# Kernel tuning notes

Measured on AMD Instinct MI355X. Metric: run time of the kernel, lower is better.

Reference implementation:

```python
import jax, jax.numpy as jnp
import numpy as np

N_NODES = 10000
N_EDGES = 640000
N_GRAPHS = 64
IN_FEAT = 128
HID = (128, 128)
NUM_CLASS = 10


def setup_inputs() -> dict:
    key = jax.random.key(0)
    ks = jax.random.split(key, 10)
    x = jax.random.normal(ks[0], (N_NODES, IN_FEAT), dtype=jnp.float32)
    edge_index = jax.random.randint(ks[1], (2, N_EDGES), 0, N_NODES, dtype=jnp.int64)
    batch = jnp.sort(jax.random.randint(ks[2], (N_NODES,), 0, N_GRAPHS, dtype=jnp.int64))
    # GCNConv weights (PyG applies x @ W then propagates, bias added after aggregation)
    s1 = 1.0 / np.sqrt(IN_FEAT)
    s2 = 1.0 / np.sqrt(HID[0])
    s3 = 1.0 / np.sqrt(HID[1])
    W1 = jax.random.uniform(ks[3], (IN_FEAT, HID[0]), jnp.float32, -s1, s1)
    b1 = jnp.zeros((HID[0],), jnp.float32)
    W2 = jax.random.uniform(ks[4], (HID[0], HID[1]), jnp.float32, -s2, s2)
    b2 = jnp.zeros((HID[1],), jnp.float32)
    Wlin = jax.random.uniform(ks[5], (HID[1], NUM_CLASS), jnp.float32, -s3, s3)
    blin = jax.random.uniform(ks[6], (NUM_CLASS,), jnp.float32, -s3, s3)
    return {"x": x, "edge_index": edge_index, "batch": batch,
            "W1": W1, "b1": b1, "W2": W2, "b2": b2, "Wlin": Wlin, "blin": blin}


def _gcn_conv(x, src, dst, W, b):
    # GCNConv with self-loops and symmetric normalization:
    # out[i] = sum_{(j->i) in E} d[j]^{-1/2} d[i]^{-1/2} (x_j W) + d[i]^{-1} (x_i W) + b
    # where d = in-degree (on dst) + 1 for the self-loop.
    h = x @ W                                                      # [N, F]
    ones = jnp.ones(src.shape[0], dtype=h.dtype)
    deg = jax.ops.segment_sum(ones, dst, num_segments=x.shape[0]) + 1.0
    dinv = jax.lax.rsqrt(deg)                                      # [N]
    norm = dinv[src] * dinv[dst]                                   # [E]
    agg = jax.ops.segment_sum(h[src] * norm[:, None], dst, num_segments=x.shape[0])
    agg = agg + h * (dinv * dinv)[:, None]                         # self-loop term
    return agg + b


def _global_mean_pool(x, batch, num_graphs):
    sums = jax.ops.segment_sum(x, batch, num_segments=num_graphs)          # [G, F]
    cnt = jax.ops.segment_sum(jnp.ones(x.shape[0], x.dtype), batch, num_segments=num_graphs)
    return sums / jnp.maximum(cnt, 1.0)[:, None]


def reference(x, edge_index, batch, W1, b1, W2, b2, Wlin, blin):
    src, dst = edge_index[0], edge_index[1]
    h = jax.nn.relu(_gcn_conv(x, src, dst, W1, b1))
    h = jax.nn.relu(_gcn_conv(h, src, dst, W2, b2))
    g = _global_mean_pool(h, batch, N_GRAPHS)      # [G, hid1]
    return g @ Wlin + blin                          # [G, num_class]
```

## Files before the change

kernel.cpp:

```cpp
#include <hip/hip_runtime.h>

#define NN 10000
#define NE 640000
#define NG 64
#define NF 128
#define NC 10
#define TMR 16
#define TKC 32
#define NB 250
#define BSZ 40
#define G1 512
#define GEMMB ((NN + TMR - 1) / TMR)
#define ECHUNK 1250
#define CAP 32
#define CCAP 3072
#define NSL 64
#define MAXD 192


__device__ __forceinline__ unsigned short f2bf(float f) {
    unsigned int u = __float_as_uint(f);
    return (unsigned short)((u + 0x7FFF + ((u >> 16) & 1)) >> 16);
}
__device__ __forceinline__ float bf_lo(unsigned int p) {
    return __uint_as_float(p << 16);
}
__device__ __forceinline__ float bf_hi(unsigned int p) {
    return __uint_as_float(p & 0xFFFF0000u);
}

__device__ __forceinline__ int detect64(const int* w, long span) {
    int lane = threadIdx.x & 63;
    long e = (long)lane * (span - 1) / 63;
    return (__ballot(w[2 * e + 1] != 0) == 0ULL) ? 1 : 0;
}

__device__ __forceinline__ int ld_idx(const void* p, long i, int is64) {
    return is64 ? (int)((const long long*)p)[i] : ((const int*)p)[i];
}

__global__ __launch_bounds__(256) void k_prepgemm(const void* __restrict__ ei,
                                                  const void* __restrict__ batch,
                                                  int* __restrict__ bh,
                                                  int* __restrict__ ebuf,
                                                  float* __restrict__ outacc,
                                                  float* __restrict__ cntinv,
                                                  const float* __restrict__ X,
                                                  const float* __restrict__ W,
                                                  unsigned short* __restrict__ Y) {
    __shared__ int hist[256];
    __shared__ int cur[256];
    __shared__ float sX[TKC * 20];
    __shared__ float sW[32 * 132];
    int tid = threadIdx.x;

    if (blockIdx.x >= G1) {
        int m0 = (int)(blockIdx.x - G1) * TMR;
        int rg = tid & 7;
        int cg = tid >> 3;
        float acc[2][4] = {{0.f}};
        for (int kc = 0; kc < NF / TKC; ++kc) {
            int k0 = kc * TKC;
            if (tid < 128) {
                int row = tid >> 3, kq = tid & 7;
                int mm = m0 + row; if (mm > NN - 1) mm = NN - 1;
                float4 v = *(const float4*)(X + (size_t)mm * NF + k0 + kq * 4);
                sX[(kq * 4 + 0) * 20 + row] = v.x;
                sX[(kq * 4 + 1) * 20 + row] = v.y;
                sX[(kq * 4 + 2) * 20 + row] = v.z;
                sX[(kq * 4 + 3) * 20 + row] = v.w;
            }
#pragma unroll
            for (int j = 0; j < 4; ++j) {
                int idx = tid + 256 * j;
                int k = idx >> 5, cq = idx & 31;
                float4 v = *(const float4*)(W + (size_t)(k0 + k) * NF + cq * 4);
                *(float4*)(sW + cq * 132 + k * 4) = v;
            }
            __syncthreads();
#pragma unroll 8
            for (int k = 0; k < TKC; ++k) {
                float2 xf = *(const float2*)(sX + k * 20 + rg * 2);
                float4 wf = *(const float4*)(sW + cg * 132 + k * 4);
                acc[0][0] = fmaf(xf.x, wf.x, acc[0][0]);
                acc[0][1] = fmaf(xf.x, wf.y, acc[0][1]);
                acc[0][2] = fmaf(xf.x, wf.z, acc[0][2]);
                acc[0][3] = fmaf(xf.x, wf.w, acc[0][3]);
                acc[1][0] = fmaf(xf.y, wf.x, acc[1][0]);
                acc[1][1] = fmaf(xf.y, wf.y, acc[1][1]);
                acc[1][2] = fmaf(xf.y, wf.z, acc[1][2]);
                acc[1][3] = fmaf(xf.y, wf.w, acc[1][3]);
            }
            __syncthreads();
        }
#pragma unroll
        for (int r = 0; r < 2; ++r) {
            int m = m0 + rg * 2 + r;
            if (m < NN) {
                ushort4 h;
                h.x = f2bf(acc[r][0]);
                h.y = f2bf(acc[r][1]);
                h.z = f2bf(acc[r][2]);
                h.w = f2bf(acc[r][3]);
                *(ushort4*)(Y + (size_t)m * NF + cg * 4) = h;
            }
        }
        return;
    }

    int is64 = detect64((const int*)ei, NE);
    hist[tid] = 0;
    __syncthreads();
    if (blockIdx.x == 0) {
        for (int i = tid; i < NSL * NG * NC; i += 256) outacc[i] = 0.f;
    }
    if (blockIdx.x == 8 && tid < NG) {
        int isb = detect64((const int*)batch, NN / 2);
        int lo0 = 0, hi0 = NN;
        while (lo0 < hi0) {
            int m = (lo0 + hi0) >> 1;
            if (ld_idx(batch, m, isb) < tid) lo0 = m + 1; else hi0 = m;
        }
        int lo1 = lo0, hi1 = NN;
        while (lo1 < hi1) {
            int m = (lo1 + hi1) >> 1;
            if (ld_idx(batch, m, isb) < tid + 1) lo1 = m + 1; else hi1 = m;
        }
        cntinv[tid] = 1.0f / fmaxf((float)(lo1 - lo0), 1.0f);
    }
    int e0 = blockIdx.x * ECHUNK;
    int dstv[5], srcv[5];
#pragma unroll
    for (int i = 0; i < 5; ++i) {
        int r = tid + i * 256;
        if (r < ECHUNK) {
            long e = (long)e0 + r;
            dstv[i] = ld_idx(ei, (long)NE + e, is64);
            srcv[i] = ld_idx(ei, e, is64);
            atomicAdd(&hist[dstv[i] / BSZ], 1);
        } else {
            dstv[i] = -1; srcv[i] = 0;
        }
    }
    __syncthreads();
    if (tid < NB) {
        bh[tid * G1 + blockIdx.x] = min(hist[tid], CAP);
        cur[tid] = (tid * G1 + blockIdx.x) * CAP;
    }
    __syncthreads();
#pragma unroll
    for (int i = 0; i < 5; ++i) {
        if (tid + i * 256 < ECHUNK) {
            int dst = dstv[i], src = srcv[i];
            int b = dst / BSZ;
            int p = atomicAdd(&cur[b], 1);
            int lim = (b * G1 + blockIdx.x) * CAP + CAP;
            if (p < lim) ebuf[p] = ((dst - b * BSZ) << 14) | src;
        }
    }
}

__global__ __launch_bounds__(256) void k_csr(const int* __restrict__ ebuf,
                                             const int* __restrict__ bh,
                                             int* __restrict__ coff,
                                             int* __restrict__ deg,
                                             float* __restrict__ dinv,
                                             unsigned short* __restrict__ csrc) {
    __shared__ int scnt[G1];
    __shared__ int cbase[G1];
    __shared__ int wsum[4];
    __shared__ int eb[CCAP];
    __shared__ int dcount[BSZ];
    __shared__ int cur[BSZ];
    int b = blockIdx.x, tid = threadIdx.x;
    int lane = tid & 63, wv = tid >> 6;
    for (int i = tid; i < G1; i += 256) scnt[i] = bh[b * G1 + i];
    if (tid < BSZ) dcount[tid] = 0;
    __syncthreads();
    int v0 = scnt[2 * tid], v1 = scnt[2 * tid + 1];
    int lsum = v0 + v1;
    int pref = lsum;
    for (int o = 1; o < 64; o <<= 1) {
        int t = __shfl_up(pref, o, 64);
        if (lane >= o) pref += t;
    }
    if (lane == 63) wsum[wv] = pref;
    __syncthreads();
    int off = 0;
#pragma unroll
    for (int j = 0; j < 4; ++j) if (j < wv) off += wsum[j];
    int ex = pref - lsum + off;
    cbase[2 * tid] = ex;
    cbase[2 * tid + 1] = ex + v0;
    int tot = wsum[0] + wsum[1] + wsum[2] + wsum[3];
    if (tot > CCAP) tot = CCAP;
    __syncthreads();
#pragma unroll
    for (int cp = 0; cp < 2; ++cp) {
        int cell = 2 * tid + cp;
        int c = scnt[cell], lb = cbase[cell];
        int gb = (b * G1 + cell) * CAP;
        if (lb + c > CCAP) c = max(0, CCAP - lb);
        for (int i = 0; i < c; ++i) eb[lb + i] = ebuf[gb + i];
    }
    __syncthreads();
    for (int i = tid; i < tot; i += 256)
        atomicAdd(&dcount[eb[i] >> 14], 1);
    __syncthreads();
    if (tid < 64) {
        int d = (tid < BSZ) ? dcount[tid] : 0;
        int pr = d;
        for (int o = 1; o < 64; o <<= 1) {
            int t = __shfl_up(pr, o, 64);
            if (tid >= o) pr += t;
        }
        if (tid < BSZ) {
            int st = pr - d;
            cur[tid] = b * CCAP + st;
            coff[b * BSZ + tid] = b * CCAP + st;
            deg[b * BSZ + tid] = d;
            dinv[b * BSZ + tid] = rsqrtf((float)d + 1.0f);
        }
    }
    __syncthreads();
    for (int i = tid; i < tot; i += 256) {
        int pk = eb[i];
        int p = atomicAdd(&cur[pk >> 14], 1);
        csrc[p] = (unsigned short)(pk & 16383);
    }
}

__global__ __launch_bounds__(256) void k_gemm(const float* __restrict__ X,
                                              const float* __restrict__ W,
                                              const float* __restrict__ dinv,
                                              unsigned short* __restrict__ Y,
                                              int nrows) {
    __shared__ float sX[TKC * 20];
    __shared__ float sW[32 * 132];
    int tid = threadIdx.x;
    int rg = tid & 7;
    int cg = tid >> 3;
    int m0 = blockIdx.x * TMR;
    float acc[2][4] = {{0.f}};
    for (int kc = 0; kc < NF / TKC; ++kc) {
        int k0 = kc * TKC;
        if (tid < 128) {
            int row = tid >> 3, kq = tid & 7;
            int mm = m0 + row; if (mm > nrows - 1) mm = nrows - 1;
            float4 v = *(const float4*)(X + (size_t)mm * NF + k0 + kq * 4);
            sX[(kq * 4 + 0) * 20 + row] = v.x;
            sX[(kq * 4 + 1) * 20 + row] = v.y;
            sX[(kq * 4 + 2) * 20 + row] = v.z;
            sX[(kq * 4 + 3) * 20 + row] = v.w;
        }
#pragma unroll
        for (int j = 0; j < 4; ++j) {
            int idx = tid + 256 * j;
            int k = idx >> 5, cq = idx & 31;
            float4 v = *(const float4*)(W + (size_t)(k0 + k) * NF + cq * 4);
            *(float4*)(sW + cq * 132 + k * 4) = v;
        }
        __syncthreads();
#pragma unroll 8
        for (int k = 0; k < TKC; ++k) {
            float2 xf = *(const float2*)(sX + k * 20 + rg * 2);
            float4 wf = *(const float4*)(sW + cg * 132 + k * 4);
            acc[0][0] = fmaf(xf.x, wf.x, acc[0][0]);
            acc[0][1] = fmaf(xf.x, wf.y, acc[0][1]);
            acc[0][2] = fmaf(xf.x, wf.z, acc[0][2]);
            acc[0][3] = fmaf(xf.x, wf.w, acc[0][3]);
            acc[1][0] = fmaf(xf.y, wf.x, acc[1][0]);
            acc[1][1] = fmaf(xf.y, wf.y, acc[1][1]);
            acc[1][2] = fmaf(xf.y, wf.z, acc[1][2]);
            acc[1][3] = fmaf(xf.y, wf.w, acc[1][3]);
        }
        __syncthreads();
    }
#pragma unroll
    for (int r = 0; r < 2; ++r) {
        int m = m0 + rg * 2 + r;
        if (m < nrows) {
            float ds = dinv[m];
            ushort4 h;
            h.x = f2bf(acc[r][0] * ds);
            h.y = f2bf(acc[r][1] * ds);
            h.z = f2bf(acc[r][2] * ds);
            h.w = f2bf(acc[r][3] * ds);
            *(ushort4*)(Y + (size_t)m * NF + cg * 4) = h;
        }
    }
}

template <int EDGE_SCALE>
__device__ __forceinline__ void gacc_node(const unsigned short* __restrict__ G,
                                          const unsigned short* __restrict__ csrc,
                                          const float* __restrict__ dv,
                                          unsigned short* ls, float* lsd,
                                          int beg, int end, int q, int f, int lane,
                                          float a[8]) {
    int dg = end - beg;
    int nst = min(dg, MAXD);
    for (int i = lane; i < nst; i += 64) {
        unsigned short s = csrc[beg + i];
        ls[i] = s;
        if (EDGE_SCALE) lsd[i] = dv[s];
    }
    int vi = q;
    int nfull = nst & ~31;
    for (; vi < nfull; vi += 32) {
        int s[8]; float d[8];
#pragma unroll
        for (int j = 0; j < 8; ++j) {
            s[j] = ls[vi + 4 * j];
            d[j] = EDGE_SCALE ? lsd[vi + 4 * j] : 1.f;
        }
        uint4 p[8];
#pragma unroll
        for (int j = 0; j < 8; ++j)
            p[j] = ((const uint4*)(G + (size_t)s[j] * NF))[f];
#pragma unroll
        for (int j = 0; j < 8; ++j) {
            if (EDGE_SCALE) {
                a[0] = fmaf(d[j], bf_lo(p[j].x), a[0]); a[1] = fmaf(d[j], bf_hi(p[j].x), a[1]);
                a[2] = fmaf(d[j], bf_lo(p[j].y), a[2]); a[3] = fmaf(d[j], bf_hi(p[j].y), a[3]);
                a[4] = fmaf(d[j], bf_lo(p[j].z), a[4]); a[5] = fmaf(d[j], bf_hi(p[j].z), a[5]);
                a[6] = fmaf(d[j], bf_lo(p[j].w), a[6]); a[7] = fmaf(d[j], bf_hi(p[j].w), a[7]);
            } else {
                a[0] += bf_lo(p[j].x); a[1] += bf_hi(p[j].x);
                a[2] += bf_lo(p[j].y); a[3] += bf_hi(p[j].y);
                a[4] += bf_lo(p[j].z); a[5] += bf_hi(p[j].z);
                a[6] += bf_lo(p[j].w); a[7] += bf_hi(p[j].w);
            }
        }
    }
    int nfull16 = nst & ~15;
    for (; vi < nfull16; vi += 16) {
        int s[4]; float d[4];
#pragma unroll
        for (int j = 0; j < 4; ++j) {
            s[j] = ls[vi + 4 * j];
            d[j] = EDGE_SCALE ? lsd[vi + 4 * j] : 1.f;
        }
        uint4 p[4];
#pragma unroll
        for (int j = 0; j < 4; ++j)
            p[j] = ((const uint4*)(G + (size_t)s[j] * NF))[f];
#pragma unroll
        for (int j = 0; j < 4; ++j) {
            if (EDGE_SCALE) {
                a[0] = fmaf(d[j], bf_lo(p[j].x), a[0]); a[1] = fmaf(d[j], bf_hi(p[j].x), a[1]);
                a[2] = fmaf(d[j], bf_lo(p[j].y), a[2]); a[3] = fmaf(d[j], bf_hi(p[j].y), a[3]);
                a[4] = fmaf(d[j], bf_lo(p[j].z), a[4]); a[5] = fmaf(d[j], bf_hi(p[j].z), a[5]);
                a[6] = fmaf(d[j], bf_lo(p[j].w), a[6]); a[7] = fmaf(d[j], bf_hi(p[j].w), a[7]);
            } else {
                a[0] += bf_lo(p[j].x); a[1] += bf_hi(p[j].x);
                a[2] += bf_lo(p[j].y); a[3] += bf_hi(p[j].y);
                a[4] += bf_lo(p[j].z); a[5] += bf_hi(p[j].z);
                a[6] += bf_lo(p[j].w); a[7] += bf_hi(p[j].w);
            }
        }
    }
    int npad = (nst + 3) & ~3;
    for (; vi < npad; vi += 4) {
        int ii = min(vi, nst - 1);
        int s = ls[ii];
        float d = EDGE_SCALE ? lsd[ii] : 1.f;
        uint4 p = ((const uint4*)(G + (size_t)s * NF))[f];
        if (vi < nst) {
            if (EDGE_SCALE) {
                a[0] = fmaf(d, bf_lo(p.x), a[0]); a[1] = fmaf(d, bf_hi(p.x), a[1]);
                a[2] = fmaf(d, bf_lo(p.y), a[2]); a[3] = fmaf(d, bf_hi(p.y), a[3]);
                a[4] = fmaf(d, bf_lo(p.z), a[4]); a[5] = fmaf(d, bf_hi(p.z), a[5]);
                a[6] = fmaf(d, bf_lo(p.w), a[6]); a[7] = fmaf(d, bf_hi(p.w), a[7]);
            } else {
                a[0] += bf_lo(p.x); a[1] += bf_hi(p.x);
                a[2] += bf_lo(p.y); a[3] += bf_hi(p.y);
                a[4] += bf_lo(p.z); a[5] += bf_hi(p.z);
                a[6] += bf_lo(p.w); a[7] += bf_hi(p.w);
            }
        }
    }
    for (int e2 = beg + MAXD + q; e2 < end; e2 += 4) {
        int s = csrc[e2];
        float d = EDGE_SCALE ? dv[s] : 1.f;
        uint4 p = ((const uint4*)(G + (size_t)s * NF))[f];
        if (EDGE_SCALE) {
            a[0] = fmaf(d, bf_lo(p.x), a[0]); a[1] = fmaf(d, bf_hi(p.x), a[1]);
            a[2] = fmaf(d, bf_lo(p.y), a[2]); a[3] = fmaf(d, bf_hi(p.y), a[3]);
            a[4] = fmaf(d, bf_lo(p.z), a[4]); a[5] = fmaf(d, bf_hi(p.z), a[5]);
            a[6] = fmaf(d, bf_lo(p.w), a[6]); a[7] = fmaf(d, bf_hi(p.w), a[7]);
        } else {
            a[0] += bf_lo(p.x); a[1] += bf_hi(p.x);
            a[2] += bf_lo(p.y); a[3] += bf_hi(p.y);
            a[4] += bf_lo(p.z); a[5] += bf_hi(p.z);
            a[6] += bf_lo(p.w); a[7] += bf_hi(p.w);
        }
    }
#pragma unroll
    for (int j = 0; j < 8; ++j) a[j] += __shfl_xor(a[j], 16);
#pragma unroll
    for (int j = 0; j < 8; ++j) a[j] += __shfl_xor(a[j], 32);
}

__global__ __launch_bounds__(256, 4) void k_gather(const unsigned short* __restrict__ G,
                                                   const int* __restrict__ off,
                                                   const int* __restrict__ dg,
                                                   const unsigned short* __restrict__ csrc,
                                                   const float* __restrict__ dinv,
                                                   const float* __restrict__ bias,
                                                   float* __restrict__ OUT) {
    __shared__ unsigned short lsbuf[4][MAXD];
    __shared__ float lsdbuf[4][MAXD];
    int wid = threadIdx.x >> 6, lane = threadIdx.x & 63;
    int q = lane >> 4, f = lane & 15;
    int n = blockIdx.x * 4 + wid;
    if (n >= NN) return;
    int beg = off[n], end = beg + dg[n];
    float din = dinv[n];
    float a[8] = {0.f, 0.f, 0.f, 0.f, 0.f, 0.f, 0.f, 0.f};
    gacc_node<1>(G, csrc, dinv, lsbuf[wid], lsdbuf[wid], beg, end, q, f, lane, a);
    if (q == 0) {
        uint4 sp = ((const uint4*)(G + (size_t)n * NF))[f];
        float4 b0 = ((const float4*)bias)[2 * f];
        float4 b1 = ((const float4*)bias)[2 * f + 1];
        float4 o0, o1;
        o0.x = fmaxf(fmaf(din, fmaf(din, bf_lo(sp.x), a[0]), b0.x), 0.f);
        o0.y = fmaxf(fmaf(din, fmaf(din, bf_hi(sp.x), a[1]), b0.y), 0.f);
        o0.z = fmaxf(fmaf(din, fmaf(din, bf_lo(sp.y), a[2]), b0.z), 0.f);
        o0.w = fmaxf(fmaf(din, fmaf(din, bf_hi(sp.y), a[3]), b0.w), 0.f);
        o1.x = fmaxf(fmaf(din, fmaf(din, bf_lo(sp.z), a[4]), b1.x), 0.f);
        o1.y = fmaxf(fmaf(din, fmaf(din, bf_hi(sp.z), a[5]), b1.y), 0.f);
        o1.z = fmaxf(fmaf(din, fmaf(din, bf_lo(sp.w), a[6]), b1.z), 0.f);
        o1.w = fmaxf(fmaf(din, fmaf(din, bf_hi(sp.w), a[7]), b1.w), 0.f);
        ((float4*)(OUT + (size_t)n * NF))[2 * f] = o0;
        ((float4*)(OUT + (size_t)n * NF))[2 * f + 1] = o1;
    }
}

__global__ __launch_bounds__(256, 4) void k_gatherpool(const unsigned short* __restrict__ G,
                                                       const int* __restrict__ off,
                                                       const int* __restrict__ dg,
                                                       const unsigned short* __restrict__ csrc,
                                                       const float* __restrict__ dinv,
                                                       const float* __restrict__ bias,
                                                       const void* __restrict__ batch,
                                                       const float* __restrict__ Wl,
                                                       const float* __restrict__ cntinv,
                                                       float* __restrict__ outacc) {
    __shared__ float sWl2[8 * NC * 16];
    __shared__ unsigned short lsbuf[4][MAXD];
    int tid = threadIdx.x;
    for (int i = tid; i < 8 * NC * 16; i += 256) {
        int j = i / (NC * 16);
        int r = i - j * (NC * 16);
        int c = r >> 4, f0 = r & 15;
        sWl2[i] = Wl[(f0 * 8 + j) * NC + c];
    }
    int isb64 = detect64((const int*)batch, NN / 2);
    int wid = tid >> 6, lane = tid & 63;
    int q = lane >> 4, f = lane & 15;
    int n = blockIdx.x * 4 + wid;
    int beg = off[n], end = beg + dg[n];
    float din = dinv[n];
    float a[8] = {0.f, 0.f, 0.f, 0.f, 0.f, 0.f, 0.f, 0.f};
    __syncthreads();
    gacc_node<0>(G, csrc, dinv, lsbuf[wid], (float*)nullptr, beg, end, q, f, lane, a);
    int g = ld_idx(batch, n, isb64);
    uint4 sp = ((const uint4*)(G + (size_t)n * NF))[f];
    float4 b0 = ((const float4*)bias)[2 * f];
    float4 b1 = ((const float4*)bias)[2 * f + 1];
    float h[8];
    h[0] = fmaxf(fmaf(din, a[0] + bf_lo(sp.x), b0.x), 0.f);
    h[1] = fmaxf(fmaf(din, a[1] + bf_hi(sp.x), b0.y), 0.f);
    h[2] = fmaxf(fmaf(din, a[2] + bf_lo(sp.y), b0.z), 0.f);
    h[3] = fmaxf(fmaf(din, a[3] + bf_hi(sp.y), b0.w), 0.f);
    h[4] = fmaxf(fmaf(din, a[4] + bf_lo(sp.z), b1.x), 0.f);
    h[5] = fmaxf(fmaf(din, a[5] + bf_hi(sp.z), b1.y), 0.f);
    h[6] = fmaxf(fmaf(din, a[6] + bf_lo(sp.w), b1.z), 0.f);
    h[7] = fmaxf(fmaf(din, a[7] + bf_hi(sp.w), b1.w), 0.f);
    float p[NC];
#pragma unroll
    for (int c = 0; c < NC; ++c) p[c] = 0.f;
#pragma unroll
    for (int j = 0; j < 8; ++j) {
        const float* wrow = sWl2 + j * (NC * 16) + f;
#pragma unroll
        for (int c = 0; c < NC; ++c) p[c] = fmaf(h[j], wrow[c * 16], p[c]);
    }
#pragma unroll
    for (int c = 0; c < NC; ++c) {
        p[c] += __shfl_xor(p[c], 1);
        p[c] += __shfl_xor(p[c], 2);
        p[c] += __shfl_xor(p[c], 4);
        p[c] += __shfl_xor(p[c], 8);
    }
    if (lane == 0) {
        float ci = cntinv[g];
        float* dst = outacc + (size_t)(blockIdx.x & (NSL - 1)) * NG * NC + g * NC;
#pragma unroll
        for (int c = 0; c < NC; ++c) atomicAdd(dst + c, p[c] * ci);
    }
}

__global__ __launch_bounds__(256) void k_fin(const float* __restrict__ outacc,
                                             const float* __restrict__ bl,
                                             float* __restrict__ out) {
    int tid = threadIdx.x;
    for (int i = tid; i < NG * NC; i += 256) {
        float s = 0.f;
#pragma unroll 8
        for (int sl = 0; sl < NSL; ++sl) s += outacc[(size_t)sl * NG * NC + i];
        out[i] = s + bl[i % NC];
    }
}

extern "C" void kernel_launch(void* const* d_in, const int* in_sizes, int n_in,
                              void* d_out, int out_size, void* d_ws, size_t ws_size,
                              hipStream_t stream) {
    const float* x  = (const float*)d_in[0];
    const void*  ei = d_in[1];
    const void*  bt = d_in[2];
    const float* W1 = (const float*)d_in[3];
    const float* b1 = (const float*)d_in[4];
    const float* W2 = (const float*)d_in[5];
    const float* b2 = (const float*)d_in[6];
    const float* Wl = (const float*)d_in[7];
    const float* bl = (const float*)d_in[8];

    char* ws = (char*)d_ws;
    int*            coff   = (int*)(ws + 0);
    int*            deg    = (int*)(ws + 40000);
    float*          dinv   = (float*)(ws + 80000);
    float*          outacc = (float*)(ws + 120000);
    float*          cntinv = (float*)(ws + 283840);
    unsigned short* csrc   = (unsigned short*)(ws + 284160);
    int*            bh     = (int*)(ws + 1820160);
    unsigned short* Gb     = (unsigned short*)(ws + 2344448);
    int*            ebuf   = (int*)(ws + 4904448);
    float*          bufB   = (float*)(ws + 4904448);

    k_prepgemm<<<G1 + GEMMB, 256, 0, stream>>>(ei, bt, bh, ebuf, outacc, cntinv,
                                               x, W1, Gb);
    k_csr <<<NB, 256, 0, stream>>>(ebuf, bh, coff, deg, dinv, csrc);

    k_gather<<<(NN + 3) / 4, 256, 0, stream>>>(Gb, coff, deg, csrc, dinv, b1, bufB);
    k_gemm<<<GEMMB, 256, 0, stream>>>(bufB, W2, dinv, Gb, NN);
    k_gatherpool<<<(NN + 3) / 4, 256, 0, stream>>>(Gb, coff, deg, csrc, dinv, b2,
                                                   bt, Wl, cntinv, outacc);
    k_fin<<<1, 256, 0, stream>>>(outacc, bl, (float*)d_out);
}
```

Baseline: 159.7 us.

## Fuse layer-1 gather with layer-2 GEMM into one kernel

The layer-1 neighbor aggregation (bias, ReLU) is merged with the W2 matrix multiply, so each wavefront computes its node's hidden row and multiplies it by W2 held in shared memory. The result is written directly as dinv-scaled bf16 into a separate buffer. This removes the fp32 intermediate write/read and one kernel launch. The cost is loading 64KB of W2 into LDS per 8-node block, a per-node shuffle-based matvec instead of a tiled GEMM, and lower occupancy from the large shared-memory footprint.

```diff
diff --git a/kernel.cpp b/kernel.cpp
--- a/kernel.cpp
+++ b/kernel.cpp
@@ -227,67 +227,6 @@
         int pk = eb[i];
         int p = atomicAdd(&cur[pk >> 14], 1);
         csrc[p] = (unsigned short)(pk & 16383);
-    }
-}
-
-__global__ __launch_bounds__(256) void k_gemm(const float* __restrict__ X,
-                                              const float* __restrict__ W,
-                                              const float* __restrict__ dinv,
-                                              unsigned short* __restrict__ Y,
-                                              int nrows) {
-    __shared__ float sX[TKC * 20];
-    __shared__ float sW[32 * 132];
-    int tid = threadIdx.x;
-    int rg = tid & 7;
-    int cg = tid >> 3;
-    int m0 = blockIdx.x * TMR;
-    float acc[2][4] = {{0.f}};
-    for (int kc = 0; kc < NF / TKC; ++kc) {
-        int k0 = kc * TKC;
-        if (tid < 128) {
-            int row = tid >> 3, kq = tid & 7;
-            int mm = m0 + row; if (mm > nrows - 1) mm = nrows - 1;
-            float4 v = *(const float4*)(X + (size_t)mm * NF + k0 + kq * 4);
-            sX[(kq * 4 + 0) * 20 + row] = v.x;
-            sX[(kq * 4 + 1) * 20 + row] = v.y;
-            sX[(kq * 4 + 2) * 20 + row] = v.z;
-            sX[(kq * 4 + 3) * 20 + row] = v.w;
-        }
-#pragma unroll
-        for (int j = 0; j < 4; ++j) {
-            int idx = tid + 256 * j;
-            int k = idx >> 5, cq = idx & 31;
-            float4 v = *(const float4*)(W + (size_t)(k0 + k) * NF + cq * 4);
-            *(float4*)(sW + cq * 132 + k * 4) = v;
-        }
-        __syncthreads();
-#pragma unroll 8
-        for (int k = 0; k < TKC; ++k) {
-            float2 xf = *(const float2*)(sX + k * 20 + rg * 2);
-            float4 wf = *(const float4*)(sW + cg * 132 + k * 4);
-            acc[0][0] = fmaf(xf.x, wf.x, acc[0][0]);
-            acc[0][1] = fmaf(xf.x, wf.y, acc[0][1]);
-            acc[0][2] = fmaf(xf.x, wf.z, acc[0][2]);
-            acc[0][3] = fmaf(xf.x, wf.w, acc[0][3]);
-            acc[1][0] = fmaf(xf.y, wf.x, acc[1][0]);
-            acc[1][1] = fmaf(xf.y, wf.y, acc[1][1]);
-            acc[1][2] = fmaf(xf.y, wf.z, acc[1][2]);
-            acc[1][3] = fmaf(xf.y, wf.w, acc[1][3]);
-        }
-        __syncthreads();
-    }
-#pragma unroll
-    for (int r = 0; r < 2; ++r) {
-        int m = m0 + rg * 2 + r;
-        if (m < nrows) {
-            float ds = dinv[m];
-            ushort4 h;
-            h.x = f2bf(acc[r][0] * ds);
-            h.y = f2bf(acc[r][1] * ds);
-            h.z = f2bf(acc[r][2] * ds);
-            h.w = f2bf(acc[r][3] * ds);
-            *(ushort4*)(Y + (size_t)m * NF + cg * 4) = h;
-        }
     }
 }
 
@@ -402,38 +341,71 @@
     for (int j = 0; j < 8; ++j) a[j] += __shfl_xor(a[j], 32);
 }
 
-__global__ __launch_bounds__(256, 4) void k_gather(const unsigned short* __restrict__ G,
-                                                   const int* __restrict__ off,
-                                                   const int* __restrict__ dg,
-                                                   const unsigned short* __restrict__ csrc,
-                                                   const float* __restrict__ dinv,
-                                                   const float* __restrict__ bias,
-                                                   float* __restrict__ OUT) {
-    __shared__ unsigned short lsbuf[4][MAXD];
-    __shared__ float lsdbuf[4][MAXD];
-    int wid = threadIdx.x >> 6, lane = threadIdx.x & 63;
+__global__ __launch_bounds__(512, 4) void k_gatherg2(const unsigned short* __restrict__ G,
+                                                     const int* __restrict__ off,
+                                                     const int* __restrict__ dg,
+                                                     const unsigned short* __restrict__ csrc,
+                                                     const float* __restrict__ dinv,
+                                                     const float* __restrict__ bias,
+                                                     const float* __restrict__ W2,
+                                                     unsigned short* __restrict__ Y) {
+    __shared__ float sW2[NF * 130];
+    __shared__ unsigned short lsbuf[8][MAXD];
+    __shared__ float lsdbuf[8][MAXD];
+    int tid = threadIdx.x;
+#pragma unroll
+    for (int it = 0; it < 8; ++it) {
+        int m = (tid + it * 512) * 4;
+        int k = m >> 7, c = m & 127;
+        float4 v = *(const float4*)(W2 + m);
+        *(float4*)(&sW2[k * 130 + c]) = v;
+    }
+    int wid = tid >> 6, lane = tid & 63;
     int q = lane >> 4, f = lane & 15;
-    int n = blockIdx.x * 4 + wid;
-    if (n >= NN) return;
+    int n = blockIdx.x * 8 + wid;
     int beg = off[n], end = beg + dg[n];
     float din = dinv[n];
     float a[8] = {0.f, 0.f, 0.f, 0.f, 0.f, 0.f, 0.f, 0.f};
+    __syncthreads();
     gacc_node<1>(G, csrc, dinv, lsbuf[wid], lsdbuf[wid], beg, end, q, f, lane, a);
+    uint4 sp = ((const uint4*)(G + (size_t)n * NF))[f];
+    float4 b0 = ((const float4*)bias)[2 * f];
+    float4 b1 = ((const float4*)bias)[2 * f + 1];
+    float h[8];
+    h[0] = fmaxf(fmaf(din, fmaf(din, bf_lo(sp.x), a[0]), b0.x), 0.f);
+    h[1] = fmaxf(fmaf(din, fmaf(din, bf_hi(sp.x), a[1]), b0.y), 0.f);
+    h[2] = fmaxf(fmaf(din, fmaf(din, bf_lo(sp.y), a[2]), b0.z), 0.f);
+    h[3] = fmaxf(fmaf(din, fmaf(din, bf_hi(sp.y), a[3]), b0.w), 0.f);
+    h[4] = fmaxf(fmaf(din, fmaf(din, bf_lo(sp.z), a[4]), b1.x), 0.f);
+    h[5] = fmaxf(fmaf(din, fmaf(din, bf_hi(sp.z), a[5]), b1.y), 0.f);
+    h[6] = fmaxf(fmaf(din, fmaf(din, bf_lo(sp.w), a[6]), b1.z), 0.f);
+    h[7] = fmaxf(fmaf(din, fmaf(din, bf_hi(sp.w), a[7]), b1.w), 0.f);
+    float o[8] = {0.f, 0.f, 0.f, 0.f, 0.f, 0.f, 0.f, 0.f};
+#pragma unroll
+    for (int kk = 0; kk < 32; ++kk) {
+        int k = q * 32 + kk;
+        float hh = __shfl(h[kk & 7], 20 * q + (kk >> 3), 64);
+        const float* wr = &sW2[k * 130 + f * 8];
+        float4 w0 = *(const float4*)(wr);
+        float4 w1 = *(const float4*)(wr + 4);
+        o[0] = fmaf(hh, w0.x, o[0]); o[1] = fmaf(hh, w0.y, o[1]);
+        o[2] = fmaf(hh, w0.z, o[2]); o[3] = fmaf(hh, w0.w, o[3]);
+        o[4] = fmaf(hh, w1.x, o[4]); o[5] = fmaf(hh, w1.y, o[5]);
+        o[6] = fmaf(hh, w1.z, o[6]); o[7] = fmaf(hh, w1.w, o[7]);
+    }
+#pragma unroll
+    for (int j = 0; j < 8; ++j) {
+        o[j] += __shfl_xor(o[j], 16);
+        o[j] += __shfl_xor(o[j], 32);
+    }
     if (q == 0) {
-        uint4 sp = ((const uint4*)(G + (size_t)n * NF))[f];
-        float4 b0 = ((const float4*)bias)[2 * f];
-        float4 b1 = ((const float4*)bias)[2 * f + 1];
-        float4 o0, o1;
-        o0.x = fmaxf(fmaf(din, fmaf(din, bf_lo(sp.x), a[0]), b0.x), 0.f);
-        o0.y = fmaxf(fmaf(din, fmaf(din, bf_hi(sp.x), a[1]), b0.y), 0.f);
-        o0.z = fmaxf(fmaf(din, fmaf(din, bf_lo(sp.y), a[2]), b0.z), 0.f);
-        o0.w = fmaxf(fmaf(din, fmaf(din, bf_hi(sp.y), a[3]), b0.w), 0.f);
-        o1.x = fmaxf(fmaf(din, fmaf(din, bf_lo(sp.z), a[4]), b1.x), 0.f);
-        o1.y = fmaxf(fmaf(din, fmaf(din, bf_hi(sp.z), a[5]), b1.y), 0.f);
-        o1.z = fmaxf(fmaf(din, fmaf(din, bf_lo(sp.w), a[6]), b1.z), 0.f);
-        o1.w = fmaxf(fmaf(din, fmaf(din, bf_hi(sp.w), a[7]), b1.w), 0.f);
-        ((float4*)(OUT + (size_t)n * NF))[2 * f] = o0;
-        ((float4*)(OUT + (size_t)n * NF))[2 * f + 1] = o1;
+        ushort4 y0, y1;
+        y0.x = f2bf(o[0] * din); y0.y = f2bf(o[1] * din);
+        y0.z = f2bf(o[2] * din); y0.w = f2bf(o[3] * din);
+        y1.x = f2bf(o[4] * din); y1.y = f2bf(o[5] * din);
+        y1.z = f2bf(o[6] * din); y1.w = f2bf(o[7] * din);
+        *(ushort4*)(Y + (size_t)n * NF + f * 8) = y0;
+        *(ushort4*)(Y + (size_t)n * NF + f * 8 + 4) = y1;
     }
 }
 
@@ -537,15 +509,14 @@
     int*            bh     = (int*)(ws + 1820160);
     unsigned short* Gb     = (unsigned short*)(ws + 2344448);
     int*            ebuf   = (int*)(ws + 4904448);
-    float*          bufB   = (float*)(ws + 4904448);
+    unsigned short* Gb2    = (unsigned short*)(ws + 4904448);
 
     k_prepgemm<<<G1 + GEMMB, 256, 0, stream>>>(ei, bt, bh, ebuf, outacc, cntinv,
                                                x, W1, Gb);
     k_csr <<<NB, 256, 0, stream>>>(ebuf, bh, coff, deg, dinv, csrc);
 
-    k_gather<<<(NN + 3) / 4, 256, 0, stream>>>(Gb, coff, deg, csrc, dinv, b1, bufB);
-    k_gemm<<<GEMMB, 256, 0, stream>>>(bufB, W2, dinv, Gb, NN);
-    k_gatherpool<<<(NN + 3) / 4, 256, 0, stream>>>(Gb, coff, deg, csrc, dinv, b2,
+    k_gatherg2<<<NN / 8, 512, 0, stream>>>(Gb, coff, deg, csrc, dinv, b1, W2, Gb2);
+    k_gatherpool<<<(NN + 3) / 4, 256, 0, stream>>>(Gb2, coff, deg, csrc, dinv, b2,
                                                    bt, Wl, cntinv, outacc);
     k_fin<<<1, 256, 0, stream>>>(outacc, bl, (float*)d_out);
 }
```

New measurement: 187.0 us. 1.17x slower.
